# Kernel tuning notes

Hardware: AMD Instinct MI355X
Metric: run time of the kernel (lower is better)

The kernel has to match this reference:

```python
import jax, jax.numpy as jnp
import numpy as np

DEPTH = 17                 # levels of the complete binary tree
N = 2**DEPTH - 1           # 131071 nodes, BFS order: children of n are 2n+1, 2n+2
IN_DIM = 128
HID = 128
OUT = 128


def setup_inputs() -> dict:
    key = jax.random.key(0)
    ks = jax.random.split(key, 20)

    def lin_w(k, o, i):
        s = 1.0 / np.sqrt(i)
        return jax.random.uniform(k, (o, i), minval=-s, maxval=s, dtype=jnp.float32)

    def lin_b(k, o, i):
        s = 1.0 / np.sqrt(i)
        return jax.random.uniform(k, (o,), minval=-s, maxval=s, dtype=jnp.float32)

    inp = {"x": jax.random.normal(ks[0], (N, IN_DIM), dtype=jnp.float32)}
    # complete binary tree, parent -> child edges (row0=src/parent, row1=dst/child)
    child = np.arange(1, N)
    parent = (child - 1) // 2
    inp["edge_index"] = jnp.asarray(np.stack([parent, child]), dtype=jnp.int32)
    names = [("Wi", "bWi", IN_DIM), ("Ui", "bUi", HID),
             ("Wf", "bWf", IN_DIM), ("Uf", "bUf", HID),
             ("Wo", "bWo", IN_DIM), ("Uo", "bUo", HID),
             ("Wu", "bWu", IN_DIM), ("Uu", "bUu", HID)]
    ki = 1
    for wname, bname, idim in names:
        inp[wname] = lin_w(ks[ki], HID, idim)
        inp[bname] = lin_b(ks[ki + 1], HID, idim)
        ki += 2
    inp["Wp"] = lin_w(ks[17], OUT, HID)
    inp["bWp"] = lin_b(ks[18], OUT, HID)
    return inp


def reference(x, edge_index, Wi, bWi, Ui, bUi, Wf, bWf, Uf, bUf,
              Wo, bWo, Uo, bUo, Wu, bWu, Uu, bUu, Wp, bWp):
    # edge_index encodes the complete binary tree in BFS order (children of n
    # are 2n+1 and 2n+2), so the recursion batches exactly by tree level.
    # Precompute input-side gate projections for ALL nodes in 4 GEMMs
    # (equivalent to calling W_*(x[node]) per node in the torch recursion).
    xi = x @ Wi.T + bWi            # (N, H)
    xf = x @ Wf.T + bWf
    xo = x @ Wo.T + bWo
    xu = x @ Wu.T + bWu

    h_next = None  # hidden states of the level below (children)
    c_next = None
    for d in range(DEPTH - 1, -1, -1):   # bottom-up over tree levels
        s = 2**d - 1                     # first node index of level d
        cnt = 2**d                       # nodes at level d
        li, lf, lo, lu = xi[s:s + cnt], xf[s:s + cnt], xo[s:s + cnt], xu[s:s + cnt]
        if h_next is None:               # leaves: no children, h_sum = 0
            i = jax.nn.sigmoid(li)
            o = jax.nn.sigmoid(lo)
            u = jnp.tanh(lu)
            c = i * u
        else:
            # children of node s+k are at positions 2(s+k)+1, 2(s+k)+2: contiguous
            ch_h = h_next.reshape(cnt, 2, HID)
            ch_c = c_next.reshape(cnt, 2, HID)
            h_sum = ch_h.sum(axis=1)     # child-sum
            i = jax.nn.sigmoid(li + h_sum @ Ui.T + bUi)
            o = jax.nn.sigmoid(lo + h_sum @ Uo.T + bUo)
            u = jnp.tanh(lu + h_sum @ Uu.T + bUu)
            # per-child forget gates: sigmoid(W_f x + U_f h_k)
            f = jax.nn.sigmoid(lf[:, None, :] + jnp.einsum('nkh,gh->nkg', ch_h, Uf) + bUf)
            c = i * u + (f * ch_c).sum(axis=1)
        h = o * jnp.tanh(c)
        h_next, c_next = h, c

    h_root = h_next[0]                   # root node index 0
    # dropout is identity in eval mode
    return h_root @ Wp.T + bWp           # (OUT,)
```

## Files before the change

kernel.cpp:

```cpp
#include <hip/hip_runtime.h>
#include <hip/hip_bf16.h>


#define DEPTH 17
#define NTREE ((1 << DEPTH) - 1)
#define DIM 128
#define XSTR 136
#define HSTR 136
#define CSTR 132

typedef __attribute__((ext_vector_type(8))) short short8;
typedef __attribute__((ext_vector_type(4))) float float4v;

__device__ __forceinline__ float sigm(float v) {
    return __fdividef(1.0f, 1.0f + __expf(-v));
}
__device__ __forceinline__ float ftanh(float v) {
    v = fminf(15.0f, fmaxf(-15.0f, v));
    float e = __expf(2.0f * v);
    return __fdividef(e - 1.0f, e + 1.0f);
}

__device__ __forceinline__ unsigned short f2bf(float f) {
    union { float f; unsigned u; } a; a.f = f;
    unsigned u = a.u;
    return (unsigned short)((u + 0x7fffu + ((u >> 16) & 1u)) >> 16);
}
__device__ __forceinline__ float bf2f(unsigned short s) {
    union { unsigned u; float f; } a; a.u = ((unsigned)s) << 16;
    return a.f;
}

struct WPtrs {
    const float* W[4];  const float* U[4];
    const float* bW[4]; const float* bU[4];
};

__global__ __launch_bounds__(256) void prep_kernel(WPtrs p, unsigned short* __restrict__ Bsw,
                                                   float* __restrict__ biasWU, float* __restrict__ biasL) {
    int idx = blockIdx.x * 256 + threadIdx.x;
    int j = idx & 7;
    int lane = (idx >> 3) & 63;
    int g = (idx >> 9) & 3;
    int ks = (idx >> 11) & 7;
    int w = idx >> 14;
    int L = lane & 15, q = lane >> 4;
    int c = w * 16 + L;
    int k = ks * 32 + q * 8 + j;
    float v = (k < 128) ? p.W[g][c * 128 + k] * (g == 3 ? 1.0f : 0.5f)
                        : p.U[g][c * 128 + (k - 128)];
    Bsw[idx] = f2bf(v);
    if (idx < 512) {
        int gg = idx >> 7, cc = idx & 127;
        biasWU[idx] = p.bW[gg][cc] + p.bU[gg][cc];
        biasL[idx]  = p.bW[gg][cc];
    }
}

template <bool LEAF0>
__global__ __launch_bounds__(512, 2) void kd2p_kernel(
    const float* __restrict__ x, const unsigned short* __restrict__ Bsw,
    const float* __restrict__ biasL, const float* __restrict__ biasWU,
    unsigned short* __restrict__ hbf, float* __restrict__ cbuf,
    int x0base, int x1base, int ntiles) {
    __shared__ __align__(16) unsigned short xs[48 * XSTR];
    __shared__ __align__(16) unsigned short hc[LEAF0 ? 16 : 64 * XSTR];
    __shared__ __align__(16) unsigned short h0[32 * XSTR];
    __shared__ __align__(16) unsigned short c0[32 * XSTR];
    __shared__ __align__(16) unsigned short hA1[16 * XSTR];
    __shared__ __align__(16) float cA1[16 * CSTR];

    const int tid = threadIdx.x;
    const int w = tid >> 6, lane = tid & 63, L = lane & 15, q = lane >> 4;
    const int ch = w * 16 + L;

    short8 b[32];
#pragma unroll
    for (int t = 0; t < 32; ++t)
        b[t] = *(const short8*)(Bsw + ((size_t)w << 14) + (t << 9) + lane * 8);

    float4 pfx[3];
    {
        const long tt = blockIdx.x;
        const long n0 = (long)x0base + tt * 32, n1 = (long)x1base + tt * 16;
#pragma unroll
        for (int k = 0; k < 3; ++k) {
            const int i = tid + 512 * k;
            const int row = i >> 5, j = i & 31;
            const long node = (row < 32) ? (n0 + row) : (n1 + (row - 32));
            pfx[k] = *(const float4*)(x + (size_t)node * DIM + j * 4);
        }
    }

    for (int it = 0; it < ntiles; ++it) {
        const long tt = (long)it * gridDim.x + blockIdx.x;
        const long n0 = (long)x0base + tt * 32;
        const long n1 = (long)x1base + tt * 16;
        const long cb = 2 * n0 + 1;

#pragma unroll
        for (int k = 0; k < 3; ++k) {
            const int i = tid + 512 * k;
            const int row = i >> 5, j = i & 31;
            ushort4 o;
            o.x = f2bf(pfx[k].x); o.y = f2bf(pfx[k].y);
            o.z = f2bf(pfx[k].z); o.w = f2bf(pfx[k].w);
            *(ushort4*)(xs + row * XSTR + j * 4) = o;
        }
        if (!LEAF0) {
            for (int i = tid; i < 64 * 16; i += 512) {
                const int row = i >> 4, g = i & 15;
                *(uint4*)(hc + row * XSTR + g * 8) =
                    *(const uint4*)(hbf + (size_t)(cb + row) * DIM + g * 8);
            }
        }
        __syncthreads();

        if (it + 1 < ntiles) {
            const long tn = tt + gridDim.x;
            const long m0 = (long)x0base + tn * 32, m1 = (long)x1base + tn * 16;
#pragma unroll
            for (int k = 0; k < 3; ++k) {
                const int i = tid + 512 * k;
                const int row = i >> 5, j = i & 31;
                const long node = (row < 32) ? (m0 + row) : (m1 + (row - 32));
                pfx[k] = *(const float4*)(x + (size_t)node * DIM + j * 4);
            }
        }

        if (LEAF0) {
            float4v acc[2][3];
#pragma unroll
            for (int mm = 0; mm < 2; ++mm)
#pragma unroll
                for (int g = 0; g < 3; ++g) acc[mm][g] = (float4v){0.f, 0.f, 0.f, 0.f};
#pragma unroll
            for (int ks = 0; ks < 4; ++ks) {
                short8 a[2];
                a[0] = *(const short8*)(xs + L * XSTR + ks * 32 + q * 8);
                a[1] = *(const short8*)(xs + (16 + L) * XSTR + ks * 32 + q * 8);
#pragma unroll
                for (int g = 0; g < 3; ++g)
#pragma unroll
                    for (int mm = 0; mm < 2; ++mm)
                        acc[mm][g] = __builtin_amdgcn_mfma_f32_16x16x32_bf16(a[mm], b[ks * 4 + g], acc[mm][g], 0, 0, 0);
            }
#pragma unroll
            for (int mm = 0; mm < 2; ++mm)
#pragma unroll
                for (int r = 0; r < 4; ++r) {
                    const int nl = 16 * mm + q * 4 + r;
                    float iv = sigm(2.f * acc[mm][0][r] + biasL[ch]);
                    float ov = sigm(2.f * acc[mm][1][r] + biasL[128 + ch]);
                    float uv = ftanh(2.f * acc[mm][2][r] + biasL[256 + ch]);
                    float cv = iv * uv;
                    c0[nl * XSTR + ch] = f2bf(cv);
                    h0[nl * XSTR + ch] = f2bf(ov * ftanh(cv));
                }
        } else {
            for (int mc = 0; mc < 4; mc += 2) {
                float4v acc[2][4];
#pragma unroll
                for (int mm = 0; mm < 2; ++mm)
#pragma unroll
                    for (int g = 0; g < 4; ++g) acc[mm][g] = (float4v){0.f, 0.f, 0.f, 0.f};
#pragma unroll
                for (int ks = 0; ks < 8; ++ks) {
                    const int kk = ks * 32;
                    short8 a[2];
#pragma unroll
                    for (int mm = 0; mm < 2; ++mm) {
                        if (kk < 128)
                            a[mm] = *(const short8*)(xs + (8 * (mc + mm) + (L >> 1)) * XSTR + kk + q * 8);
                        else
                            a[mm] = *(const short8*)(hc + (16 * (mc + mm) + L) * XSTR + (kk - 128) + q * 8);
                    }
#pragma unroll
                    for (int g = 0; g < 4; ++g)
#pragma unroll
                        for (int mm = 0; mm < 2; ++mm)
                            acc[mm][g] = __builtin_amdgcn_mfma_f32_16x16x32_bf16(a[mm], b[ks * 4 + g], acc[mm][g], 0, 0, 0);
                }
#pragma unroll
                for (int mm = 0; mm < 2; ++mm)
#pragma unroll
                    for (int e = 0; e < 2; ++e) {
                        const int nl = 8 * (mc + mm) + 2 * q + e;
                        const int r0 = 2 * e, r1 = 2 * e + 1;
                        float iv = sigm(acc[mm][0][r0] + acc[mm][0][r1] + biasWU[ch]);
                        float ov = sigm(acc[mm][1][r0] + acc[mm][1][r1] + biasWU[128 + ch]);
                        float uv = ftanh(acc[mm][2][r0] + acc[mm][2][r1] + biasWU[256 + ch]);
                        float fl = sigm(acc[mm][3][r0] + biasWU[384 + ch]);
                        float fr = sigm(acc[mm][3][r1] + biasWU[384 + ch]);
                        float cl = cbuf[(size_t)(cb + 2 * nl) * DIM + ch];
                        float cr = cbuf[(size_t)(cb + 2 * nl + 1) * DIM + ch];
                        float cv = iv * uv + fl * cl + fr * cr;
                        c0[nl * XSTR + ch] = f2bf(cv);
                        h0[nl * XSTR + ch] = f2bf(ov * ftanh(cv));
                    }
            }
        }
        __syncthreads();

        {
            float4v acc[2][4];
#pragma unroll
            for (int mm = 0; mm < 2; ++mm)
#pragma unroll
                for (int g = 0; g < 4; ++g) acc[mm][g] = (float4v){0.f, 0.f, 0.f, 0.f};
#pragma unroll
            for (int ks = 0; ks < 8; ++ks) {
                const int kk = ks * 32;
                short8 a[2];
#pragma unroll
                for (int mm = 0; mm < 2; ++mm) {
                    if (kk < 128)
                        a[mm] = *(const short8*)(xs + (32 + 8 * mm + (L >> 1)) * XSTR + kk + q * 8);
                    else
                        a[mm] = *(const short8*)(h0 + (16 * mm + L) * XSTR + (kk - 128) + q * 8);
                }
#pragma unroll
                for (int g = 0; g < 4; ++g)
#pragma unroll
                    for (int mm = 0; mm < 2; ++mm)
                        acc[mm][g] = __builtin_amdgcn_mfma_f32_16x16x32_bf16(a[mm], b[ks * 4 + g], acc[mm][g], 0, 0, 0);
            }
#pragma unroll
            for (int mm = 0; mm < 2; ++mm)
#pragma unroll
                for (int e = 0; e < 2; ++e) {
                    const int nl = 8 * mm + 2 * q + e;
                    const int r0 = 2 * e, r1 = 2 * e + 1;
                    float iv = sigm(acc[mm][0][r0] + acc[mm][0][r1] + biasWU[ch]);
                    float ov = sigm(acc[mm][1][r0] + acc[mm][1][r1] + biasWU[128 + ch]);
                    float uv = ftanh(acc[mm][2][r0] + acc[mm][2][r1] + biasWU[256 + ch]);
                    float fl = sigm(acc[mm][3][r0] + biasWU[384 + ch]);
                    float fr = sigm(acc[mm][3][r1] + biasWU[384 + ch]);
                    float cl = bf2f(c0[(2 * nl) * XSTR + ch]);
                    float cr = bf2f(c0[(2 * nl + 1) * XSTR + ch]);
                    float cv = iv * uv + fl * cl + fr * cr;
                    cA1[nl * CSTR + ch] = cv;
                    hA1[nl * XSTR + ch] = f2bf(ov * ftanh(cv));
                }
        }
        __syncthreads();

        for (int i = tid; i < 16 * 16; i += 512) {
            const int row = i >> 4, g = i & 15;
            *(uint4*)(hbf + (size_t)(n1 + row) * DIM + g * 8) = *(const uint4*)(hA1 + row * XSTR + g * 8);
        }
        for (int i = tid; i < 16 * 32; i += 512) {
            const int row = i >> 5, j = i & 31;
            *(float4*)(cbuf + (size_t)(n1 + row) * DIM + j * 4) = *(const float4*)(cA1 + row * CSTR + j * 4);
        }
    }
}

template <bool GCH>
__device__ __forceinline__ void internal_level(
    const unsigned short* xc,
    const unsigned short* hin_l, const float* cin_l,
    const unsigned short* __restrict__ hin_g, const float* __restrict__ cin_g, long cb,
    unsigned short* ho, int ho_str, float* co, int co_str, int cnt,
    const short8 (&b)[32], const float* __restrict__ biasWU,
    int L, int q, int ch) {
    const int rows = 2 * cnt;
    const int mt = (rows + 15) >> 4;
    for (int mc = 0; mc < mt; mc += 2) {
        const int mm_n = (mt - mc >= 2) ? 2 : 1;
        float4v acc[2][4];
#pragma unroll
        for (int mm = 0; mm < 2; ++mm)
#pragma unroll
            for (int g = 0; g < 4; ++g) acc[mm][g] = (float4v){0.f, 0.f, 0.f, 0.f};
#pragma unroll
        for (int ks = 0; ks < 8; ++ks) {
            const int kk = ks * 32;
            short8 a[2];
#pragma unroll
            for (int mm = 0; mm < 2; ++mm) {
                if (mm < mm_n) {
                    if (kk < 128) {
                        int xr = 8 * (mc + mm) + (L >> 1);
                        if (xr >= cnt) xr = 0;
                        a[mm] = *(const short8*)(xc + xr * XSTR + kk + q * 8);
                    } else if (!GCH) {
                        a[mm] = *(const short8*)(hin_l + (16 * (mc + mm) + L) * HSTR + (kk - 128) + q * 8);
                    } else {
                        a[mm] = *(const short8*)(hin_g + (size_t)(cb + 16 * (mc + mm) + L) * DIM + (kk - 128) + q * 8);
                    }
                }
            }
#pragma unroll
            for (int g = 0; g < 4; ++g)
#pragma unroll
                for (int mm = 0; mm < 2; ++mm)
                    if (mm < mm_n)
                        acc[mm][g] = __builtin_amdgcn_mfma_f32_16x16x32_bf16(a[mm], b[ks * 4 + g], acc[mm][g], 0, 0, 0);
        }
#pragma unroll
        for (int mm = 0; mm < 2; ++mm)
#pragma unroll
            for (int e = 0; e < 2; ++e) {
                if (mm < mm_n) {
                    const int nl = 8 * (mc + mm) + 2 * q + e;
                    if (nl < cnt) {
                        const int r0 = 2 * e, r1 = 2 * e + 1;
                        float iv = sigm(acc[mm][0][r0] + acc[mm][0][r1] + biasWU[ch]);
                        float ov = sigm(acc[mm][1][r0] + acc[mm][1][r1] + biasWU[128 + ch]);
                        float uv = ftanh(acc[mm][2][r0] + acc[mm][2][r1] + biasWU[256 + ch]);
                        float fl = sigm(acc[mm][3][r0] + biasWU[384 + ch]);
                        float fr = sigm(acc[mm][3][r1] + biasWU[384 + ch]);
                        float cl, cr;
                        if (!GCH) {
                            cl = cin_l[(2 * nl) * CSTR + ch];
                            cr = cin_l[(2 * nl + 1) * CSTR + ch];
                        } else {
                            cl = cin_g[(size_t)(cb + 2 * nl) * DIM + ch];
                            cr = cin_g[(size_t)(cb + 2 * nl + 1) * DIM + ch];
                        }
                        float cv = iv * uv + fl * cl + fr * cr;
                        co[nl * co_str + ch] = cv;
                        ho[nl * ho_str + ch] = f2bf(ov * ftanh(cv));
                    }
                }
            }
    }
}

template <int C, int NL, bool PROJ>
__global__ __launch_bounds__(512, 2) void k23_kernel(
    const float* __restrict__ x, const unsigned short* __restrict__ Bsw,
    const float* __restrict__ biasWU, unsigned short* __restrict__ hbf,
    float* __restrict__ cbuf, int d0,
    const float* __restrict__ Wp, const float* __restrict__ bWp,
    float* __restrict__ out) {
    constexpr int TOTX = 2 * C - (C >> (NL - 1));
    constexpr int AR = (C < 16) ? 16 : C;
    __shared__ __align__(16) unsigned short xs[TOTX * XSTR];
    __shared__ __align__(16) unsigned short hA[AR * HSTR];
    __shared__ __align__(16) unsigned short hB[16 * HSTR];
    __shared__ __align__(16) float cA[AR * CSTR];
    __shared__ __align__(16) float cB[16 * CSTR];
    __shared__ float red[4][128];

    const int tid = threadIdx.x;
    const int w = tid >> 6, lane = tid & 63, L = lane & 15, q = lane >> 4;
    const int ch = w * 16 + L;

    short8 b[32];
#pragma unroll
    for (int t = 0; t < 32; ++t)
        b[t] = *(const short8*)(Bsw + ((size_t)w << 14) + (t << 9) + lane * 8);

    {
        int xoff = 0;
#pragma unroll
        for (int l = 0; l < NL; ++l) {
            const int rows = C >> l;
            const long base = ((1 << (d0 - l)) - 1) + (long)blockIdx.x * rows;
            for (int i = tid; i < rows * 32; i += 512) {
                const int row = i >> 5, j = i & 31;
                float4 v = *(const float4*)(x + (size_t)(base + row) * DIM + j * 4);
                ushort4 o;
                o.x = f2bf(v.x); o.y = f2bf(v.y); o.z = f2bf(v.z); o.w = f2bf(v.w);
                *(ushort4*)(xs + (xoff + row) * XSTR + j * 4) = o;
            }
            xoff += rows;
        }
    }
    __syncthreads();

    const long cb = ((1 << (d0 + 1)) - 1) + (long)blockIdx.x * (2 * C);
    internal_level<true>(xs, nullptr, nullptr, hbf, cbuf, cb,
                         hA, HSTR, cA, CSTR, C, b, biasWU, L, q, ch);
    __syncthreads();

    const unsigned short* hin = hA;
    const float* cin = cA;
    int xoff = C;
#pragma unroll
    for (int l = 1; l < NL; ++l) {
        const int cnt = C >> l;
        if (!PROJ && l == NL - 1) {
            const long ob = ((1 << (d0 - (NL - 1))) - 1) + (long)blockIdx.x;
            internal_level<false>(xs + xoff * XSTR, hin, cin, nullptr, nullptr, 0,
                                  hbf + (size_t)ob * DIM, DIM,
                                  cbuf + (size_t)ob * DIM, DIM, cnt, b, biasWU, L, q, ch);
        } else {
            unsigned short* ho = (l & 1) ? hB : hA;
            float* co = (l & 1) ? cB : cA;
            internal_level<false>(xs + xoff * XSTR, hin, cin, nullptr, nullptr, 0,
                                  ho, HSTR, co, CSTR, cnt, b, biasWU, L, q, ch);
            __syncthreads();
            hin = ho; cin = co;
        }
        xoff += cnt;
    }

    if (PROJ) {
        const int o = tid & 127, sg = tid >> 7;
        float pacc = 0.f;
#pragma unroll
        for (int jj = 0; jj < 8; ++jj) {
            const int k = sg * 32 + jj * 4;
            float4 wv = *(const float4*)(Wp + o * DIM + k);
            pacc += bf2f(hin[k]) * wv.x + bf2f(hin[k + 1]) * wv.y +
                    bf2f(hin[k + 2]) * wv.z + bf2f(hin[k + 3]) * wv.w;
        }
        red[sg][o] = pacc;
        __syncthreads();
        if (tid < 128) out[tid] = bWp[tid] + red[0][tid] + red[1][tid] + red[2][tid] + red[3][tid];
    }
}

extern "C" void kernel_launch(void* const* d_in, const int* in_sizes, int n_in,
                              void* d_out, int out_size, void* d_ws, size_t ws_size,
                              hipStream_t stream) {
    const float* x   = (const float*)d_in[0];
    const float* Wi  = (const float*)d_in[2];  const float* bWi = (const float*)d_in[3];
    const float* Ui  = (const float*)d_in[4];  const float* bUi = (const float*)d_in[5];
    const float* Wf  = (const float*)d_in[6];  const float* bWf = (const float*)d_in[7];
    const float* Uf  = (const float*)d_in[8];  const float* bUf = (const float*)d_in[9];
    const float* Wo  = (const float*)d_in[10]; const float* bWo = (const float*)d_in[11];
    const float* Uo  = (const float*)d_in[12]; const float* bUo = (const float*)d_in[13];
    const float* Wu  = (const float*)d_in[14]; const float* bWu = (const float*)d_in[15];
    const float* Uu  = (const float*)d_in[16]; const float* bUu = (const float*)d_in[17];
    const float* Wp  = (const float*)d_in[18]; const float* bWp = (const float*)d_in[19];

    unsigned short* Bsw = (unsigned short*)d_ws;
    float* biasWU = (float*)(Bsw + 131072);
    float* biasL  = biasWU + 512;
    float* cbuf   = biasL + 512;
    unsigned short* hbf = (unsigned short*)(cbuf + (size_t)65536 * DIM);

    WPtrs p;
    p.W[0] = Wi; p.W[1] = Wo; p.W[2] = Wu; p.W[3] = Wf;
    p.U[0] = Ui; p.U[1] = Uo; p.U[2] = Uu; p.U[3] = Uf;
    p.bW[0] = bWi; p.bW[1] = bWo; p.bW[2] = bWu; p.bW[3] = bWf;
    p.bU[0] = bUi; p.bU[1] = bUo; p.bU[2] = bUu; p.bU[3] = bUf;

    prep_kernel<<<512, 256, 0, stream>>>(p, Bsw, biasWU, biasL);

    kd2p_kernel<true><<<256, 512, 0, stream>>>(x, Bsw, biasL, biasWU, hbf, cbuf,
                                               (1 << 16) - 1, (1 << 15) - 1, 8);
    kd2p_kernel<false><<<256, 512, 0, stream>>>(x, Bsw, biasL, biasWU, hbf, cbuf,
                                                (1 << 14) - 1, (1 << 13) - 1, 2);
    kd2p_kernel<false><<<128, 512, 0, stream>>>(x, Bsw, biasL, biasWU, hbf, cbuf,
                                                (1 << 12) - 1, (1 << 11) - 1, 1);
    k23_kernel<32, 6, false><<<32, 512, 0, stream>>>(x, Bsw, biasWU, hbf, cbuf, 10,
                                                     nullptr, nullptr, nullptr);
    k23_kernel<16, 5, true><<<1, 512, 0, stream>>>(x, Bsw, biasWU, hbf, cbuf, 4,
                                                   Wp, bWp, (float*)d_out);
}
```

Baseline: 242.6 us.

## Add software-pipelined leaf-level kernel overlapping x prefetch, leaf and parent compute

Replaces the leaf-level two-level kernel with a new kd2f kernel. It prefetches the next tile's x rows into registers while the current tile is processed, and double-buffers the leaf h/c and parent x tiles in shared memory. The parent-level MFMA work for the previous tile is interleaved with the leaf computation of the current tile. The aim is to hide global load latency and cut barrier stalls between the two stages, at the cost of more registers and shared memory, which may reduce occupancy.

After: 254.0 us. +4.7%, slower.

```diff
diff --git a/kernel.cpp b/kernel.cpp
--- a/kernel.cpp
+++ b/kernel.cpp
@@ -54,6 +54,183 @@
         int gg = idx >> 7, cc = idx & 127;
         biasWU[idx] = p.bW[gg][cc] + p.bU[gg][cc];
         biasL[idx]  = p.bW[gg][cc];
+    }
+}
+
+__device__ __forceinline__ void l1_compute(
+    const unsigned short* xs1p, const unsigned short* h0p, const unsigned short* c0p,
+    unsigned short* hA1, float* cA1,
+    const short8 (&b)[24], const unsigned short* __restrict__ bfbase,
+    const float* __restrict__ biasWU, int L, int q, int ch) {
+    float4v acc[2][4];
+#pragma unroll
+    for (int mm = 0; mm < 2; ++mm)
+#pragma unroll
+        for (int g = 0; g < 4; ++g) acc[mm][g] = (float4v){0.f, 0.f, 0.f, 0.f};
+#pragma unroll
+    for (int ks = 0; ks < 8; ++ks) {
+        const int kk = ks * 32;
+        short8 a[2];
+#pragma unroll
+        for (int mm = 0; mm < 2; ++mm) {
+            if (kk < 128)
+                a[mm] = *(const short8*)(xs1p + (8 * mm + (L >> 1)) * XSTR + kk + q * 8);
+            else
+                a[mm] = *(const short8*)(h0p + (16 * mm + L) * XSTR + (kk - 128) + q * 8);
+        }
+        const short8 bf = *(const short8*)(bfbase + ((size_t)ks << 11));
+#pragma unroll
+        for (int g = 0; g < 3; ++g)
+#pragma unroll
+            for (int mm = 0; mm < 2; ++mm)
+                acc[mm][g] = __builtin_amdgcn_mfma_f32_16x16x32_bf16(a[mm], b[ks * 3 + g], acc[mm][g], 0, 0, 0);
+#pragma unroll
+        for (int mm = 0; mm < 2; ++mm)
+            acc[mm][3] = __builtin_amdgcn_mfma_f32_16x16x32_bf16(a[mm], bf, acc[mm][3], 0, 0, 0);
+    }
+#pragma unroll
+    for (int mm = 0; mm < 2; ++mm)
+#pragma unroll
+        for (int e = 0; e < 2; ++e) {
+            const int nl = 8 * mm + 2 * q + e;
+            const int r0 = 2 * e, r1 = 2 * e + 1;
+            float iv = sigm(acc[mm][0][r0] + acc[mm][0][r1] + biasWU[ch]);
+            float ov = sigm(acc[mm][1][r0] + acc[mm][1][r1] + biasWU[128 + ch]);
+            float uv = ftanh(acc[mm][2][r0] + acc[mm][2][r1] + biasWU[256 + ch]);
+            float fl = sigm(acc[mm][3][r0] + biasWU[384 + ch]);
+            float fr = sigm(acc[mm][3][r1] + biasWU[384 + ch]);
+            float cl = bf2f(c0p[(2 * nl) * XSTR + ch]);
+            float cr = bf2f(c0p[(2 * nl + 1) * XSTR + ch]);
+            float cv = iv * uv + fl * cl + fr * cr;
+            cA1[nl * CSTR + ch] = cv;
+            hA1[nl * XSTR + ch] = f2bf(ov * ftanh(cv));
+        }
+}
+
+__global__ __launch_bounds__(512, 2) void kd2f_kernel(
+    const float* __restrict__ x, const unsigned short* __restrict__ Bsw,
+    const float* __restrict__ biasL, const float* __restrict__ biasWU,
+    unsigned short* __restrict__ hbf, float* __restrict__ cbuf,
+    int x0base, int x1base, int ntiles) {
+    __shared__ __align__(16) unsigned short xs0[32 * XSTR];
+    __shared__ __align__(16) unsigned short xs1[2][16 * XSTR];
+    __shared__ __align__(16) unsigned short h0[2][32 * XSTR];
+    __shared__ __align__(16) unsigned short c0[2][32 * XSTR];
+    __shared__ __align__(16) unsigned short hA1[16 * XSTR];
+    __shared__ __align__(16) float cA1[16 * CSTR];
+
+    const int tid = threadIdx.x;
+    const int w = tid >> 6, lane = tid & 63, L = lane & 15, q = lane >> 4;
+    const int ch = w * 16 + L;
+
+    short8 b[24];
+#pragma unroll
+    for (int ks = 0; ks < 8; ++ks)
+#pragma unroll
+        for (int g = 0; g < 3; ++g)
+            b[ks * 3 + g] = *(const short8*)(Bsw + ((size_t)w << 14) + ((size_t)(ks * 4 + g) << 9) + lane * 8);
+    const unsigned short* bfbase = Bsw + ((size_t)w << 14) + (3 << 9) + lane * 8;
+
+    float4 pfx[3];
+    {
+        const long tt = blockIdx.x;
+        const long n0 = (long)x0base + tt * 32, n1 = (long)x1base + tt * 16;
+#pragma unroll
+        for (int k = 0; k < 3; ++k) {
+            const int i = tid + 512 * k;
+            const int row = i >> 5, j = i & 31;
+            const long node = (k < 2) ? (n0 + row) : (n1 + (row - 32));
+            pfx[k] = *(const float4*)(x + (size_t)node * DIM + j * 4);
+        }
+    }
+
+    for (int it = 0; it < ntiles; ++it) {
+        const long tt = (long)it * gridDim.x + blockIdx.x;
+        const int pc = it & 1;
+
+#pragma unroll
+        for (int k = 0; k < 3; ++k) {
+            const int i = tid + 512 * k;
+            const int row = i >> 5, j = i & 31;
+            ushort4 o;
+            o.x = f2bf(pfx[k].x); o.y = f2bf(pfx[k].y);
+            o.z = f2bf(pfx[k].z); o.w = f2bf(pfx[k].w);
+            if (k < 2)
+                *(ushort4*)(xs0 + row * XSTR + j * 4) = o;
+            else
+                *(ushort4*)(xs1[pc] + (row - 32) * XSTR + j * 4) = o;
+        }
+        __syncthreads();
+
+        if (it + 1 < ntiles) {
+            const long tn = tt + gridDim.x;
+            const long m0 = (long)x0base + tn * 32, m1 = (long)x1base + tn * 16;
+#pragma unroll
+            for (int k = 0; k < 3; ++k) {
+                const int i = tid + 512 * k;
+                const int row = i >> 5, j = i & 31;
+                const long node = (k < 2) ? (m0 + row) : (m1 + (row - 32));
+                pfx[k] = *(const float4*)(x + (size_t)node * DIM + j * 4);
+            }
+        }
+
+        if (it > 0)
+            l1_compute(xs1[pc ^ 1], h0[pc ^ 1], c0[pc ^ 1], hA1, cA1,
+                       b, bfbase, biasWU, L, q, ch);
+
+#pragma unroll
+        for (int mm = 0; mm < 2; ++mm) {
+            float4v acc[3];
+#pragma unroll
+            for (int g = 0; g < 3; ++g) acc[g] = (float4v){0.f, 0.f, 0.f, 0.f};
+#pragma unroll
+            for (int ks = 0; ks < 4; ++ks) {
+                short8 a = *(const short8*)(xs0 + (16 * mm + L) * XSTR + ks * 32 + q * 8);
+#pragma unroll
+                for (int g = 0; g < 3; ++g)
+                    acc[g] = __builtin_amdgcn_mfma_f32_16x16x32_bf16(a, b[ks * 3 + g], acc[g], 0, 0, 0);
+            }
+#pragma unroll
+            for (int r = 0; r < 4; ++r) {
+                const int nl = 16 * mm + q * 4 + r;
+                float iv = sigm(2.f * acc[0][r] + biasL[ch]);
+                float ov = sigm(2.f * acc[1][r] + biasL[128 + ch]);
+                float uv = ftanh(2.f * acc[2][r] + biasL[256 + ch]);
+                float cv = iv * uv;
+                c0[pc][nl * XSTR + ch] = f2bf(cv);
+                h0[pc][nl * XSTR + ch] = f2bf(ov * ftanh(cv));
+            }
+        }
+        __syncthreads();
+
+        if (it > 0) {
+            const long pn1 = (long)x1base + (tt - gridDim.x) * 16;
+            for (int i = tid; i < 16 * 16; i += 512) {
+                const int row = i >> 4, g = i & 15;
+                *(uint4*)(hbf + (size_t)(pn1 + row) * DIM + g * 8) = *(const uint4*)(hA1 + row * XSTR + g * 8);
+            }
+            for (int i = tid; i < 16 * 32; i += 512) {
+                const int row = i >> 5, j = i & 31;
+                *(float4*)(cbuf + (size_t)(pn1 + row) * DIM + j * 4) = *(const float4*)(cA1 + row * CSTR + j * 4);
+            }
+        }
+    }
+
+    __syncthreads();
+    {
+        const long tl = (long)(ntiles - 1) * gridDim.x + blockIdx.x;
+        const int pl = (ntiles - 1) & 1;
+        l1_compute(xs1[pl], h0[pl], c0[pl], hA1, cA1, b, bfbase, biasWU, L, q, ch);
+        __syncthreads();
+        const long n1 = (long)x1base + tl * 16;
+        for (int i = tid; i < 16 * 16; i += 512) {
+            const int row = i >> 4, g = i & 15;
+            *(uint4*)(hbf + (size_t)(n1 + row) * DIM + g * 8) = *(const uint4*)(hA1 + row * XSTR + g * 8);
+        }
+        for (int i = tid; i < 16 * 32; i += 512) {
+            const int row = i >> 5, j = i & 31;
+            *(float4*)(cbuf + (size_t)(n1 + row) * DIM + j * 4) = *(const float4*)(cA1 + row * CSTR + j * 4);
+        }
     }
 }
 
@@ -442,8 +619,8 @@
 
     prep_kernel<<<512, 256, 0, stream>>>(p, Bsw, biasWU, biasL);
 
-    kd2p_kernel<true><<<256, 512, 0, stream>>>(x, Bsw, biasL, biasWU, hbf, cbuf,
-                                               (1 << 16) - 1, (1 << 15) - 1, 8);
+    kd2f_kernel<<<256, 512, 0, stream>>>(x, Bsw, biasL, biasWU, hbf, cbuf,
+                                         (1 << 16) - 1, (1 << 15) - 1, 8);
     kd2p_kernel<false><<<256, 512, 0, stream>>>(x, Bsw, biasL, biasWU, hbf, cbuf,
                                                 (1 << 14) - 1, (1 << 13) - 1, 2);
     kd2p_kernel<false><<<128, 512, 0, stream>>>(x, Bsw, biasL, biasWU, hbf, cbuf,
```

## Double-buffer x tile and defer h/c stores to remove per-tile barrier

Applied to the files above, without the earlier changes.

The x staging buffer becomes double-buffered so the end-of-tile __syncthreads can be dropped. The global write-back of each tile's level-1 h/c results is moved into the next iteration, after that iteration's barrier, and the last tile is written after the loop. f2bf is also switched to the compiler's native __bf16 conversion, which may map to a hardware convert instruction. This saves one block barrier per tile in exchange for more LDS use, and it depends on the hA1/h0/c0 reuse still being ordered correctly by the single remaining barrier.

Result: no change. 243.3 us (+0.3%).

```diff
diff --git a/kernel.cpp b/kernel.cpp
--- a/kernel.cpp
+++ b/kernel.cpp
@@ -22,9 +22,10 @@
 }
 
 __device__ __forceinline__ unsigned short f2bf(float f) {
-    union { float f; unsigned u; } a; a.f = f;
-    unsigned u = a.u;
-    return (unsigned short)((u + 0x7fffu + ((u >> 16) & 1u)) >> 16);
+    __bf16 h = (__bf16)f;
+    unsigned short r;
+    __builtin_memcpy(&r, &h, 2);
+    return r;
 }
 __device__ __forceinline__ float bf2f(unsigned short s) {
     union { unsigned u; float f; } a; a.u = ((unsigned)s) << 16;
@@ -58,12 +59,12 @@
 }
 
 template <bool LEAF0>
-__global__ __launch_bounds__(512, 2) void kd2p_kernel(
+__global__ __launch_bounds__(512, 2) void kd2r_kernel(
     const float* __restrict__ x, const unsigned short* __restrict__ Bsw,
     const float* __restrict__ biasL, const float* __restrict__ biasWU,
     unsigned short* __restrict__ hbf, float* __restrict__ cbuf,
     int x0base, int x1base, int ntiles) {
-    __shared__ __align__(16) unsigned short xs[48 * XSTR];
+    __shared__ __align__(16) unsigned short xs[2][48 * XSTR];
     __shared__ __align__(16) unsigned short hc[LEAF0 ? 16 : 64 * XSTR];
     __shared__ __align__(16) unsigned short h0[32 * XSTR];
     __shared__ __align__(16) unsigned short c0[32 * XSTR];
@@ -97,6 +98,8 @@
         const long n0 = (long)x0base + tt * 32;
         const long n1 = (long)x1base + tt * 16;
         const long cb = 2 * n0 + 1;
+        const int pc = it & 1;
+        unsigned short* xsp = xs[pc];
 
 #pragma unroll
         for (int k = 0; k < 3; ++k) {
@@ -105,7 +108,7 @@
             ushort4 o;
             o.x = f2bf(pfx[k].x); o.y = f2bf(pfx[k].y);
             o.z = f2bf(pfx[k].z); o.w = f2bf(pfx[k].w);
-            *(ushort4*)(xs + row * XSTR + j * 4) = o;
+            *(ushort4*)(xsp + row * XSTR + j * 4) = o;
         }
         if (!LEAF0) {
             for (int i = tid; i < 64 * 16; i += 512) {
@@ -128,6 +131,18 @@
             }
         }
 
+        if (it > 0) {
+            const long pn1 = n1 - (long)gridDim.x * 16;
+            for (int i = tid; i < 16 * 16; i += 512) {
+                const int row = i >> 4, g = i & 15;
+                *(uint4*)(hbf + (size_t)(pn1 + row) * DIM + g * 8) = *(const uint4*)(hA1 + row * XSTR + g * 8);
+            }
+            for (int i = tid; i < 16 * 32; i += 512) {
+                const int row = i >> 5, j = i & 31;
+                *(float4*)(cbuf + (size_t)(pn1 + row) * DIM + j * 4) = *(const float4*)(cA1 + row * CSTR + j * 4);
+            }
+        }
+
         if (LEAF0) {
             float4v acc[2][3];
 #pragma unroll
@@ -137,8 +152,8 @@
 #pragma unroll
             for (int ks = 0; ks < 4; ++ks) {
                 short8 a[2];
-                a[0] = *(const short8*)(xs + L * XSTR + ks * 32 + q * 8);
-                a[1] = *(const short8*)(xs + (16 + L) * XSTR + ks * 32 + q * 8);
+                a[0] = *(const short8*)(xsp + L * XSTR + ks * 32 + q * 8);
+                a[1] = *(const short8*)(xsp + (16 + L) * XSTR + ks * 32 + q * 8);
 #pragma unroll
                 for (int g = 0; g < 3; ++g)
 #pragma unroll
@@ -171,7 +186,7 @@
 #pragma unroll
                     for (int mm = 0; mm < 2; ++mm) {
                         if (kk < 128)
-                            a[mm] = *(const short8*)(xs + (8 * (mc + mm) + (L >> 1)) * XSTR + kk + q * 8);
+                            a[mm] = *(const short8*)(xsp + (8 * (mc + mm) + (L >> 1)) * XSTR + kk + q * 8);
                         else
                             a[mm] = *(const short8*)(hc + (16 * (mc + mm) + L) * XSTR + (kk - 128) + q * 8);
                     }
@@ -215,7 +230,7 @@
 #pragma unroll
                 for (int mm = 0; mm < 2; ++mm) {
                     if (kk < 128)
-                        a[mm] = *(const short8*)(xs + (32 + 8 * mm + (L >> 1)) * XSTR + kk + q * 8);
+                        a[mm] = *(const short8*)(xsp + (32 + 8 * mm + (L >> 1)) * XSTR + kk + q * 8);
                     else
                         a[mm] = *(const short8*)(h0 + (16 * mm + L) * XSTR + (kk - 128) + q * 8);
                 }
@@ -243,8 +258,12 @@
                     hA1[nl * XSTR + ch] = f2bf(ov * ftanh(cv));
                 }
         }
-        __syncthreads();
-
+    }
+
+    __syncthreads();
+    {
+        const long tl = (long)(ntiles - 1) * gridDim.x + blockIdx.x;
+        const long n1 = (long)x1base + tl * 16;
         for (int i = tid; i < 16 * 16; i += 512) {
             const int row = i >> 4, g = i & 15;
             *(uint4*)(hbf + (size_t)(n1 + row) * DIM + g * 8) = *(const uint4*)(hA1 + row * XSTR + g * 8);
@@ -442,11 +461,11 @@
 
     prep_kernel<<<512, 256, 0, stream>>>(p, Bsw, biasWU, biasL);
 
-    kd2p_kernel<true><<<256, 512, 0, stream>>>(x, Bsw, biasL, biasWU, hbf, cbuf,
+    kd2r_kernel<true><<<256, 512, 0, stream>>>(x, Bsw, biasL, biasWU, hbf, cbuf,
                                                (1 << 16) - 1, (1 << 15) - 1, 8);
-    kd2p_kernel<false><<<256, 512, 0, stream>>>(x, Bsw, biasL, biasWU, hbf, cbuf,
+    kd2r_kernel<false><<<256, 512, 0, stream>>>(x, Bsw, biasL, biasWU, hbf, cbuf,
                                                 (1 << 14) - 1, (1 << 13) - 1, 2);
-    kd2p_kernel<false><<<128, 512, 0, stream>>>(x, Bsw, biasL, biasWU, hbf, cbuf,
+    kd2r_kernel<false><<<128, 512, 0, stream>>>(x, Bsw, biasL, biasWU, hbf, cbuf,
                                                 (1 << 12) - 1, (1 << 11) - 1, 1);
     k23_kernel<32, 6, false><<<32, 512, 0, stream>>>(x, Bsw, biasWU, hbf, cbuf, 10,
                                                      nullptr, nullptr, nullptr);
```
